# Kernel tuning notes

Measured on AMD Instinct MI355X. Metric: run time of the kernel, lower is better.

Reference implementation:

```python
import jax, jax.numpy as jnp
import numpy as np

N = 80000
E = 1280000
EPS = 1e-5

def _lrelu(x):
    return jax.nn.leaky_relu(x, 0.01)

def _bn(h):
    # training-mode BatchNorm1d with batch size 1: stats over the node dim; affine is identity at init
    return (h - h.mean(0)) / jnp.sqrt(h.var(0) + EPS)

def _ln(h, g, b):
    m = h.mean(-1, keepdims=True)
    v = h.var(-1, keepdims=True)
    return (h - m) / jnp.sqrt(v + EPS) * g + b

def _gcn(h, w, b, src, dst, n):
    # PyG GCNConv: add self loops, symmetric deg^-1/2 normalization, aggregate at target
    hw = h @ w.T
    loop = jnp.arange(n, dtype=src.dtype)
    s = jnp.concatenate([src, loop])
    d = jnp.concatenate([dst, loop])
    deg = jax.ops.segment_sum(jnp.ones(d.shape, hw.dtype), d, num_segments=n)
    dinv = jnp.where(deg > 0, 1.0 / jnp.sqrt(deg), 0.0)
    msg = hw[s] * (dinv[s] * dinv[d])[:, None]  # [E+N, C]
    return jax.ops.segment_sum(msg, d, num_segments=n) + b

def _tnet(x, c1w, c1b, c2w, c2b, c3w, c3b, f1w, f1b, f2w, f2b, f3w, f3b):
    h = jax.nn.relu(x @ c1w.T + c1b)          # [N,64]  (source skips bn1)
    h = jax.nn.relu(_bn(h @ c2w.T + c2b))     # [N,128]
    h = jax.nn.relu(_bn(h @ c3w.T + c3b))     # [N,1024]
    g = h.max(0)                              # global max pool -> [1024]
    g = jax.nn.relu(g @ f1w.T + f1b)
    g = jax.nn.relu(g @ f2w.T + f2b)
    iden = jnp.array([1.0, 0.0, 0.0, 0.0, 1.0, 0.0, 0.0, 0.0, 1.0], x.dtype)
    g = g @ f3w.T + f3b + iden
    return g.reshape(3, 3)

def _forward(edge_index, x, tnet_c1_w, tnet_c1_b, tnet_c2_w, tnet_c2_b, tnet_c3_w, tnet_c3_b, tnet_fc1_w, tnet_fc1_b, tnet_fc2_w, tnet_fc2_b, tnet_fc3_w, tnet_fc3_b, conv1_w, conv1_b, g1_li_w, g1_li_b, g1_gcn_w, g1_gcn_b, g1_ln_g, g1_ln_b, conv2_w, conv2_b, g2_li_w, g2_li_b, g2_gcn_w, g2_gcn_b, g2_ln_g, g2_ln_b, conv3_w, conv3_b, out_w, out_b):
    src, dst = edge_index[0], edge_index[1]
    n = x.shape[0]
    T = _tnet(x, tnet_c1_w, tnet_c1_b, tnet_c2_w, tnet_c2_b, tnet_c3_w, tnet_c3_b, tnet_fc1_w, tnet_fc1_b, tnet_fc2_w, tnet_fc2_b, tnet_fc3_w, tnet_fc3_b)
    h0 = x @ T                                  # [N,3] spatial transform
    xg = _lrelu(h0 @ conv1_w.T + conv1_b)       # [N,64] (conv1d k=1 == per-node linear)
    # Gcn_Attention 1
    nf = _lrelu(xg @ g1_li_w.T + g1_li_b)
    nf2 = _lrelu(_gcn(nf, g1_gcn_w, g1_gcn_b, src, dst, n))
    h = _ln(jnp.concatenate([nf, nf2], 1), g1_ln_g, g1_ln_b)   # [N,128]
    h = _lrelu(h @ conv2_w.T + conv2_b)
    # Gcn_Attention 2
    nf = _lrelu(h @ g2_li_w.T + g2_li_b)
    nf2 = _lrelu(_gcn(nf, g2_gcn_w, g2_gcn_b, src, dst, n))
    h = _ln(jnp.concatenate([nf, nf2], 1), g2_ln_g, g2_ln_b)   # [N,256]
    h = jnp.concatenate([h, xg], 1)                            # [N,320]
    h = _lrelu(h @ conv3_w.T + conv3_b)                        # [N,256]
    pooled = h.mean(0)                                         # global mean pool (single graph)
    feat = jnp.concatenate([jnp.broadcast_to(pooled, (n, pooled.shape[0])), xg], 1)  # [N,320]
    return feat @ out_w.T + out_b                              # [N,4]

def setup_inputs():
    ki = iter(jax.random.split(jax.random.key(0), 32))
    def W(shape):
        return jax.random.normal(next(ki), shape, jnp.float32) * (1.0 / float(np.sqrt(shape[-1])))
    z = lambda n: jnp.zeros((n,), jnp.float32)
    o = lambda n: jnp.ones((n,), jnp.float32)
    inp = {}
    inp['x'] = jax.random.normal(next(ki), (N, 3), jnp.float32)
    inp['edge_index'] = jax.random.randint(next(ki), (2, E), 0, N, dtype=jnp.int32)
    inp['tnet_c1_w'] = W((64, 3)); inp['tnet_c1_b'] = z(64)
    inp['tnet_c2_w'] = W((128, 64)); inp['tnet_c2_b'] = z(128)
    inp['tnet_c3_w'] = W((1024, 128)); inp['tnet_c3_b'] = z(1024)
    inp['tnet_fc1_w'] = W((512, 1024)); inp['tnet_fc1_b'] = z(512)
    inp['tnet_fc2_w'] = W((256, 512)); inp['tnet_fc2_b'] = z(256)
    inp['tnet_fc3_w'] = W((9, 256)); inp['tnet_fc3_b'] = z(9)
    inp['conv1_w'] = W((64, 3)); inp['conv1_b'] = z(64)
    inp['g1_li_w'] = W((64, 64)); inp['g1_li_b'] = z(64)
    inp['g1_gcn_w'] = W((64, 64)); inp['g1_gcn_b'] = z(64)
    inp['g1_ln_g'] = o(128); inp['g1_ln_b'] = z(128)
    inp['conv2_w'] = W((128, 128)); inp['conv2_b'] = z(128)
    inp['g2_li_w'] = W((128, 128)); inp['g2_li_b'] = z(128)
    inp['g2_gcn_w'] = W((128, 128)); inp['g2_gcn_b'] = z(128)
    inp['g2_ln_g'] = o(256); inp['g2_ln_b'] = z(256)
    inp['conv3_w'] = W((256, 320)); inp['conv3_b'] = z(256)
    inp['out_w'] = W((4, 320)); inp['out_b'] = z(4)
    return inp

def reference(x, edge_index, tnet_c1_w, tnet_c1_b, tnet_c2_w, tnet_c2_b, tnet_c3_w, tnet_c3_b, tnet_fc1_w, tnet_fc1_b, tnet_fc2_w, tnet_fc2_b, tnet_fc3_w, tnet_fc3_b, conv1_w, conv1_b, g1_li_w, g1_li_b, g1_gcn_w, g1_gcn_b, g1_ln_g, g1_ln_b, conv2_w, conv2_b, g2_li_w, g2_li_b, g2_gcn_w, g2_gcn_b, g2_ln_g, g2_ln_b, conv3_w, conv3_b, out_w, out_b):
    return _forward(edge_index, x, tnet_c1_w, tnet_c1_b, tnet_c2_w, tnet_c2_b, tnet_c3_w, tnet_c3_b, tnet_fc1_w, tnet_fc1_b, tnet_fc2_w, tnet_fc2_b, tnet_fc3_w, tnet_fc3_b, conv1_w, conv1_b, g1_li_w, g1_li_b, g1_gcn_w, g1_gcn_b, g1_ln_g, g1_ln_b, conv2_w, conv2_b, g2_li_w, g2_li_b, g2_gcn_w, g2_gcn_b, g2_ln_g, g2_ln_b, conv3_w, conv3_b, out_w, out_b)
```

## Files before the change

kernel.cpp:

```cpp
#include <hip/hip_runtime.h>
#include <cstddef>

#define EPSV 1e-5f

typedef __attribute__((ext_vector_type(8))) short frag8;
typedef __attribute__((ext_vector_type(4))) float f32x4;

__device__ __forceinline__ float lrelu01(float v) { return v > 0.f ? v : 0.01f * v; }
__device__ __forceinline__ void atomAddF(float* p, float v) { unsafeAtomicAdd(p, v); }
__device__ __forceinline__ unsigned fkey(float f) {
    unsigned u = __float_as_uint(f);
    return (u & 0x80000000u) ? ~u : (u | 0x80000000u);
}
__device__ __forceinline__ unsigned short f2b(float f) {
    unsigned u = __float_as_uint(f);
    unsigned r = u + 0x7fffu + ((u >> 16) & 1u);
    return (unsigned short)(r >> 16);
}
__device__ __forceinline__ float b2f(unsigned short h) {
    return __uint_as_float(((unsigned)h) << 16);
}
__device__ __forceinline__ float blo(unsigned u) { return __uint_as_float(u << 16); }
__device__ __forceinline__ float bhi(unsigned u) { return __uint_as_float(u & 0xffff0000u); }

static inline unsigned cdivu(unsigned a, unsigned b) { return (a + b - 1) / b; }


__global__ void k_degrank(const int* __restrict__ dst, int* __restrict__ deg,
                          int* __restrict__ rank, int E) {
    int e = blockIdx.x * 256 + threadIdx.x;
    if (e < E) rank[e] = atomicAdd(&deg[dst[e]], 1);
}

__global__ void k_scan_local(const int* __restrict__ deg, int* __restrict__ startv,
                             int* __restrict__ bsum, float* __restrict__ dinv, int n) {
    __shared__ int t0[256];
    int tid = threadIdx.x;
    int i = blockIdx.x * 256 + tid;
    int v = (i < n) ? deg[i] : 0;
    if (i < n) dinv[i] = rsqrtf((float)(v + 1));
    t0[tid] = v;
    __syncthreads();
    for (int o = 1; o < 256; o <<= 1) {
        int add = (tid >= o) ? t0[tid - o] : 0;
        __syncthreads();
        t0[tid] += add;
        __syncthreads();
    }
    if (i < n) startv[i] = t0[tid] - v;
    if (tid == 255) bsum[blockIdx.x] = t0[255];
}

__global__ void k_scan_bsum(int* __restrict__ bsum, int nb) {
    __shared__ int t0[512];
    int tid = threadIdx.x;
    int v = (tid < nb) ? bsum[tid] : 0;
    t0[tid] = v;
    __syncthreads();
    for (int o = 1; o < 512; o <<= 1) {
        int add = (tid >= o) ? t0[tid - o] : 0;
        __syncthreads();
        t0[tid] += add;
        __syncthreads();
    }
    if (tid < nb) bsum[tid] = t0[tid] - v;
}

__global__ void k_scan_add(int* __restrict__ startv, const int* __restrict__ bsum, int n) {
    int i = blockIdx.x * 256 + threadIdx.x;
    if (i < n) startv[i] += bsum[blockIdx.x];
}

__global__ void k_fill(const int* __restrict__ src, const int* __restrict__ dst,
                       const int* __restrict__ rank, const int* __restrict__ startv,
                       int* __restrict__ csr, int E) {
    int e = blockIdx.x * 256 + threadIdx.x;
    if (e < E) csr[startv[dst[e]] + rank[e]] = src[e];
}

template <int CH>
__launch_bounds__(256)
__global__ void k_gln(const int* __restrict__ startv, const int* __restrict__ degv,
                      const int* __restrict__ csr, const unsigned short* __restrict__ q,
                      const unsigned short* __restrict__ nf, const float* __restrict__ dinv,
                      const float* __restrict__ gcn_b, const float* __restrict__ lng,
                      const float* __restrict__ lnb, unsigned short* __restrict__ outp,
                      int ldo, int n) {
    const int wv = threadIdx.x >> 6, lane = threadIdx.x & 63;
    const int g = lane >> 4, p = lane & 15;
    int node = blockIdx.x * 4 + wv;
    if (node >= n) return;
    constexpr int CPL = CH / 16;
    constexpr int DPL = CPL / 2;

    float acc[CPL];
#pragma unroll
    for (int k = 0; k < CPL; ++k) acc[k] = 0.f;

    {
        unsigned su[DPL];
        const unsigned short* qrow = q + (size_t)node * CH + p * CPL;
        if (DPL == 4) *(uint4*)su = *(const uint4*)qrow;
        else          *(uint2*)su = *(const uint2*)qrow;
        if (g == 0) {
#pragma unroll
            for (int d = 0; d < DPL; ++d) { acc[2 * d] += blo(su[d]); acc[2 * d + 1] += bhi(su[d]); }
        }
    }

    int s0 = startv[node], cnt = degv[node];
    int sidx[4];
#pragma unroll
    for (int t = 0; t < 4; ++t) { int j = t * 4 + g; sidx[t] = (j < cnt) ? csr[s0 + j] : 0; }
    for (int j0 = 0; j0 < cnt; j0 += 16) {
        unsigned buf[4][DPL];
#pragma unroll
        for (int t = 0; t < 4; ++t) {
            const unsigned short* src = q + (size_t)sidx[t] * CH + p * CPL;
            if (DPL == 4) *(uint4*)buf[t] = *(const uint4*)src;
            else          *(uint2*)buf[t] = *(const uint2*)src;
        }
        int nsidx[4];
#pragma unroll
        for (int t = 0; t < 4; ++t) {
            int j = j0 + 16 + t * 4 + g;
            nsidx[t] = (j < cnt) ? csr[s0 + j] : 0;
        }
#pragma unroll
        for (int t = 0; t < 4; ++t) {
            if (j0 + t * 4 + g < cnt) {
#pragma unroll
                for (int d = 0; d < DPL; ++d) {
                    acc[2 * d] += blo(buf[t][d]);
                    acc[2 * d + 1] += bhi(buf[t][d]);
                }
            }
        }
#pragma unroll
        for (int t = 0; t < 4; ++t) sidx[t] = nsidx[t];
    }

#pragma unroll
    for (int k = 0; k < CPL; ++k) {
        acc[k] += __shfl_xor(acc[k], 16);
        acc[k] += __shfl_xor(acc[k], 32);
    }

    float di = dinv[node];
    float nv[CPL], bv[CPL];
    {
        unsigned su[DPL];
        const unsigned short* nrow = nf + (size_t)node * CH + p * CPL;
        if (DPL == 4) *(uint4*)su = *(const uint4*)nrow;
        else          *(uint2*)su = *(const uint2*)nrow;
#pragma unroll
        for (int d = 0; d < DPL; ++d) { nv[2 * d] = blo(su[d]); nv[2 * d + 1] = bhi(su[d]); }
    }
    const float* gb = gcn_b + p * CPL;
#pragma unroll
    for (int k = 0; k < CPL; ++k) bv[k] = lrelu01(di * acc[k] + gb[k]);

    float s = 0.f, ss = 0.f;
#pragma unroll
    for (int k = 0; k < CPL; ++k) { s += nv[k] + bv[k]; ss += nv[k] * nv[k] + bv[k] * bv[k]; }
#pragma unroll
    for (int off = 32; off > 0; off >>= 1) { s += __shfl_xor(s, off); ss += __shfl_xor(ss, off); }
    const float inv = 1.f / (float)(8 * CH);
    float mu = s * inv;
    float var = ss * inv - mu * mu;
    float rsg = rsqrtf(var + EPSV);

    unsigned short* orow = outp + (size_t)node * ldo;
    if (g == 0) {
        unsigned short tmp[CPL];
        const float* lg = lng + p * CPL; const float* lb = lnb + p * CPL;
#pragma unroll
        for (int k = 0; k < CPL; ++k) tmp[k] = f2b((nv[k] - mu) * rsg * lg[k] + lb[k]);
        if (DPL == 4) *(uint4*)(orow + p * CPL) = *(uint4*)tmp;
        else          *(uint2*)(orow + p * CPL) = *(uint2*)tmp;
    } else if (g == 1) {
        unsigned short tmp[CPL];
        const float* lg = lng + CH + p * CPL; const float* lb = lnb + CH + p * CPL;
#pragma unroll
        for (int k = 0; k < CPL; ++k) tmp[k] = f2b((bv[k] - mu) * rsg * lg[k] + lb[k]);
        if (DPL == 4) *(uint4*)(orow + CH + p * CPL) = *(uint4*)tmp;
        else          *(uint2*)(orow + CH + p * CPL) = *(uint2*)tmp;
    }
}


__global__ void k_wconv(const float* __restrict__ s0, const float* __restrict__ s1,
                        const float* __restrict__ s2, const float* __restrict__ s3,
                        const float* __restrict__ s4, const float* __restrict__ s5,
                        const float* __restrict__ s6, const float* __restrict__ s7,
                        unsigned short* __restrict__ dst) {
    int t = blockIdx.x * 256 + threadIdx.x;
    if (t >= 278528) return;
    const float* srcs[8] = {s0, s1, s2, s3, s4, s5, s6, s7};
    const int off[9] = {0, 8192, 139264, 143360, 147456, 163840, 180224, 196608, 278528};
    int seg = 0;
    while (t >= off[seg + 1]) ++seg;
    unsigned short v = f2b(srcs[seg][t - off[seg]]);
    if (seg == 1) {
        int li = t - 8192;
        int rch = li >> 7, k = li & 127;
        int cb = rch >> 7, r = rch & 127;
        int flat = ((r >> 4) * 4 + (k >> 5)) * 64 + ((k >> 3) & 3) * 16 + (r & 15);
        dst[8192 + cb * 16384 + flat * 8 + (k & 7)] = v;
    } else {
        dst[t] = v;
    }
}

__global__ void k_h1(const float* __restrict__ x, const float* __restrict__ w,
                     const float* __restrict__ b, unsigned short* __restrict__ h1, int n) {
    int node = blockIdx.x * 256 + threadIdx.x;
    if (node >= n) return;
    float x0 = x[node * 3], x1 = x[node * 3 + 1], x2 = x[node * 3 + 2];
    unsigned short* o = h1 + (size_t)node * 64;
#pragma unroll
    for (int cp = 0; cp < 8; ++cp) {
        unsigned short tmp[8];
#pragma unroll
        for (int t = 0; t < 8; ++t) {
            int c = cp * 8 + t;
            float v = x0 * w[c * 3] + x1 * w[c * 3 + 1] + x2 * w[c * 3 + 2] + b[c];
            tmp[t] = f2b(fmaxf(v, 0.f));
        }
        *(float4*)(o + cp * 8) = *(float4*)tmp;
    }
}

__global__ void k_prebn(const float* __restrict__ z, const float* __restrict__ sum2,
                        const float* __restrict__ ss2, unsigned short* __restrict__ a3f,
                        int n16, float invn) {
    int t = blockIdx.x * 256 + threadIdx.x;
    if (t >= n16) return;
    int row = t >> 4, cp = t & 15;
    int c = cp * 8;
    const float* src = z + (size_t)row * 128 + c;
    float4 v0 = *(const float4*)src;
    float4 v1 = *(const float4*)(src + 4);
    float vv[8] = {v0.x, v0.y, v0.z, v0.w, v1.x, v1.y, v1.z, v1.w};
    unsigned short o[8];
#pragma unroll
    for (int i = 0; i < 8; ++i) {
        float m = sum2[c + i] * invn;
        float var = ss2[c + i] * invn - m * m;
        o[i] = f2b(fmaxf((vv[i] - m) * rsqrtf(var + EPSV), 0.f));
    }
    int tile = row >> 7, r = row & 127;
    int flat = ((r >> 4) * 4 + (cp >> 2)) * 64 + (cp & 3) * 16 + (r & 15);
    *(float4*)(a3f + (size_t)tile * 16384 + flat * 8) = *(float4*)o;
}

__launch_bounds__(256)
__global__ void k_fc1(const float* __restrict__ sum3, const float* __restrict__ ss3,
                      const unsigned* __restrict__ maxk,
                      const float* __restrict__ f1w, const float* __restrict__ f1b,
                      float* __restrict__ a1, float invn) {
    __shared__ float g[1024];
    int tid = threadIdx.x;
    for (int c = tid; c < 1024; c += 256) {
        float m = sum3[c] * invn;
        float var = ss3[c] * invn - m * m;
        unsigned k = maxk[c];
        unsigned u = (k & 0x80000000u) ? (k & 0x7FFFFFFFu) : ~k;
        g[c] = fmaxf((__uint_as_float(u) - m) * rsqrtf(var + EPSV), 0.f);
    }
    __syncthreads();
    int row = blockIdx.x * 64 + (tid >> 2);
    int part = tid & 3;
    const float* w = f1w + (size_t)row * 1024 + part * 256;
    const float* gg = g + part * 256;
    float s = 0.f;
    for (int k = 0; k < 256; ++k) s = fmaf(w[k], gg[k], s);
    s += __shfl_xor(s, 1); s += __shfl_xor(s, 2);
    if (part == 0) a1[row] = fmaxf(s + f1b[row], 0.f);
}

__launch_bounds__(256)
__global__ void k_fc23(const float* __restrict__ a1, const float* __restrict__ f2w,
                       const float* __restrict__ f2b, const float* __restrict__ f3w,
                       const float* __restrict__ f3b, float* __restrict__ T9) {
    __shared__ float a2[256];
    int tid = threadIdx.x;
    {
        const float* w = f2w + (size_t)tid * 512;
        float s = f2b[tid];
        for (int k = 0; k < 512; ++k) s = fmaf(w[k], a1[k], s);
        a2[tid] = fmaxf(s, 0.f);
    }
    __syncthreads();
    if (tid < 9) {
        const float* w = f3w + (size_t)tid * 256;
        float s = f3b[tid];
        for (int k = 0; k < 256; ++k) s = fmaf(w[k], a2[k], s);
        if (tid == 0 || tid == 4 || tid == 8) s += 1.f;
        T9[tid] = s;
    }
}

__global__ void k_xg(const float* __restrict__ x, const float* __restrict__ T9,
                     const float* __restrict__ w, const float* __restrict__ b,
                     unsigned short* __restrict__ xg, int n) {
    int node = blockIdx.x * 256 + threadIdx.x;
    if (node >= n) return;
    float x0 = x[node * 3], x1 = x[node * 3 + 1], x2 = x[node * 3 + 2];
    float h0 = x0 * T9[0] + x1 * T9[3] + x2 * T9[6];
    float h1 = x0 * T9[1] + x1 * T9[4] + x2 * T9[7];
    float h2 = x0 * T9[2] + x1 * T9[5] + x2 * T9[8];
    unsigned short* o = xg + (size_t)node * 320;
#pragma unroll
    for (int cp = 0; cp < 8; ++cp) {
        unsigned short tmp[8];
#pragma unroll
        for (int t = 0; t < 8; ++t) {
            int c = cp * 8 + t;
            float v = h0 * w[c * 3] + h1 * w[c * 3 + 1] + h2 * w[c * 3 + 2] + b[c];
            tmp[t] = f2b(lrelu01(v));
        }
        *(float4*)(o + cp * 8) = *(float4*)tmp;
    }
}

__global__ void k_const4(const float* __restrict__ pooled, const float* __restrict__ ow,
                         const float* __restrict__ ob, float* __restrict__ c4, float invn) {
    int j = threadIdx.x >> 6, lane = threadIdx.x & 63;
    float s = 0.f;
    for (int c = lane; c < 256; c += 64) s += pooled[c] * invn * ow[j * 320 + c];
#pragma unroll
    for (int off = 32; off > 0; off >>= 1) s += __shfl_down(s, off);
    if (lane == 0) c4[j] = s + ob[j];
}

__global__ void k_out(const unsigned short* __restrict__ hcat, const float* __restrict__ ow,
                      const float* __restrict__ c4, float* __restrict__ out, int n) {
    int node = blockIdx.x * 256 + threadIdx.x;
    if (node >= n) return;
    const unsigned short* xgp = hcat + (size_t)node * 320 + 256;
    float s0 = c4[0], s1 = c4[1], s2 = c4[2], s3 = c4[3];
#pragma unroll
    for (int cp = 0; cp < 8; ++cp) {
        float4 raw = *(const float4*)(xgp + cp * 8);
        unsigned short tmp[8];
        *(float4*)tmp = raw;
#pragma unroll
        for (int t = 0; t < 8; ++t) {
            int k = 256 + cp * 8 + t;
            float f = b2f(tmp[t]);
            s0 = fmaf(f, ow[k], s0);
            s1 = fmaf(f, ow[320 + k], s1);
            s2 = fmaf(f, ow[640 + k], s2);
            s3 = fmaf(f, ow[960 + k], s3);
        }
    }
    *(float4*)(out + (size_t)node * 4) = make_float4(s0, s1, s2, s3);
}

enum { MF_BIAS = 1, MF_LRELU = 2, MF_DINV = 4, MF_STOREF = 8, MF_STOREB = 16,
       MF_STATS = 32, MF_COLSUM = 64 };

template <int BN, int MODE>
__launch_bounds__(256)
__global__ void k_mgemm(const unsigned short* __restrict__ A, int lda, int K,
                        const unsigned short* __restrict__ W,
                        const float* __restrict__ bias,
                        float* __restrict__ OutF, unsigned short* __restrict__ OutB, int ldo,
                        const float* __restrict__ dinv,
                        float* __restrict__ sum_o, float* __restrict__ ss_o,
                        unsigned* __restrict__ maxk_o) {
    constexpr int BM = 128;
    constexpr int LDT = 40;
    __shared__ unsigned short As[BM * LDT];
    __shared__ unsigned short Ws[BN * LDT];
    __shared__ float redS[2 * 128];
    __shared__ unsigned redM[128];

    const int tid = threadIdx.x;
    const int wid = tid >> 6, lane = tid & 63;
    const int quad = lane >> 4, lrow = lane & 15;
    const int bn0 = blockIdx.x * BM;
    const int bc0 = blockIdx.y * BN;

    constexpr int NI = (BN == 128) ? 4 : 2;
    constexpr int NJ = 4;
    const int wm = (BN == 128) ? (wid & 1) * 64 : wid * 32;
    const int wn = (BN == 128) ? (wid >> 1) * 64 : 0;

    if (MODE & (MF_STATS | MF_COLSUM)) {
        for (int c = tid; c < BN; c += 256) {
            redS[c] = 0.f; redS[128 + c] = 0.f; redM[c] = 0u;
        }
    }

    f32x4 acc[NI][NJ] = {};

    for (int k0 = 0; k0 < K; k0 += 32) {
#pragma unroll
        for (int h = 0; h < 2; ++h) {
            int ch = tid + h * 256;
            int row = ch >> 2, cp = ch & 3;
            const unsigned short* src = A + (size_t)(bn0 + row) * lda + k0 + cp * 8;
            *(float4*)&As[row * LDT + cp * 8] = *(const float4*)src;
        }
#pragma unroll
        for (int h = 0; h < BN / 64; ++h) {
            int ch = tid + h * 256;
            int row = ch >> 2, cp = ch & 3;
            const unsigned short* src = W + (size_t)(bc0 + row) * K + k0 + cp * 8;
            *(float4*)&Ws[row * LDT + cp * 8] = *(const float4*)src;
        }
        __syncthreads();
        frag8 af[NI], bf[NJ];
#pragma unroll
        for (int i = 0; i < NI; ++i)
            af[i] = *(const frag8*)&As[(wm + i * 16 + lrow) * LDT + quad * 8];
#pragma unroll
        for (int j = 0; j < NJ; ++j)
            bf[j] = *(const frag8*)&Ws[(wn + j * 16 + lrow) * LDT + quad * 8];
#pragma unroll
        for (int i = 0; i < NI; ++i)
#pragma unroll
            for (int j = 0; j < NJ; ++j)
                acc[i][j] = __builtin_amdgcn_mfma_f32_16x16x32_bf16(af[i], bf[j], acc[i][j], 0, 0, 0);
        __syncthreads();
    }

#pragma unroll
    for (int j = 0; j < NJ; ++j) {
        const int col = bc0 + wn + j * 16 + lrow;
        float bv = (MODE & MF_BIAS) ? bias[col] : 0.f;
        float s = 0.f, q = 0.f, m = -3.4e38f;
#pragma unroll
        for (int i = 0; i < NI; ++i) {
            const int rowb = bn0 + wm + i * 16 + quad * 4;
#pragma unroll
            for (int r = 0; r < 4; ++r) {
                float t = acc[i][j][r] + bv;
                if (MODE & MF_LRELU) t = lrelu01(t);
                if (MODE & MF_DINV) t *= dinv[rowb + r];
                if (MODE & MF_STOREF) OutF[(size_t)(rowb + r) * ldo + col] = t;
                if (MODE & MF_STOREB) OutB[(size_t)(rowb + r) * ldo + col] = f2b(t);
                s += t; q += t * t; m = fmaxf(m, t);
            }
        }
        if (MODE & (MF_STATS | MF_COLSUM)) {
            s += __shfl_xor(s, 16); s += __shfl_xor(s, 32);
            if (MODE & MF_STATS) {
                q += __shfl_xor(q, 16); q += __shfl_xor(q, 32);
                m = fmaxf(m, __shfl_xor(m, 16)); m = fmaxf(m, __shfl_xor(m, 32));
            }
            if (quad == 0) {
                int lc = wn + j * 16 + lrow;
                atomicAdd(&redS[lc], s);
                if (MODE & MF_STATS) {
                    atomicAdd(&redS[128 + lc], q);
                    atomicMax(&redM[lc], fkey(m));
                }
            }
        }
    }
    if (MODE & (MF_STATS | MF_COLSUM)) {
        __syncthreads();
        for (int c = tid; c < BN; c += 256) {
            atomAddF(&sum_o[bc0 + c], redS[c]);
            if (MODE & MF_STATS) {
                atomAddF(&ss_o[bc0 + c], redS[128 + c]);
                atomicMax(&maxk_o[bc0 + c], redM[c]);
            }
        }
    }
}

template <int BN>
__launch_bounds__(256)
__global__ void k_ligc(const unsigned short* __restrict__ A, int lda, int K,
                       const unsigned short* __restrict__ Wli, const float* __restrict__ bli,
                       const unsigned short* __restrict__ Wgc, const float* __restrict__ dinv,
                       unsigned short* __restrict__ NF, int ldnf,
                       unsigned short* __restrict__ Q, int ldq) {
    constexpr int BM = 128;
    constexpr int LDT = 40;
    constexpr int LDT2 = BN + 8;
    __shared__ unsigned short SA[BM * LDT2];
    __shared__ unsigned short Ws[BN * LDT];

    const int tid = threadIdx.x;
    const int wid = tid >> 6, lane = tid & 63;
    const int quad = lane >> 4, lrow = lane & 15;
    const int bn0 = blockIdx.x * BM;
    constexpr int NI = (BN == 128) ? 4 : 2;
    constexpr int NJ = 4;
    const int wm = (BN == 128) ? (wid & 1) * 64 : wid * 32;
    const int wn = (BN == 128) ? (wid >> 1) * 64 : 0;

    {
        f32x4 acc[NI][NJ] = {};
        for (int k0 = 0; k0 < K; k0 += 32) {
#pragma unroll
            for (int h = 0; h < 2; ++h) {
                int ch = tid + h * 256;
                int row = ch >> 2, cp = ch & 3;
                *(float4*)&SA[row * LDT + cp * 8] =
                    *(const float4*)(A + (size_t)(bn0 + row) * lda + k0 + cp * 8);
            }
#pragma unroll
            for (int h = 0; h < BN / 64; ++h) {
                int ch = tid + h * 256;
                int row = ch >> 2, cp = ch & 3;
                *(float4*)&Ws[row * LDT + cp * 8] =
                    *(const float4*)(Wli + (size_t)row * K + k0 + cp * 8);
            }
            __syncthreads();
            frag8 af[NI], bf[NJ];
#pragma unroll
            for (int i = 0; i < NI; ++i)
                af[i] = *(const frag8*)&SA[(wm + i * 16 + lrow) * LDT + quad * 8];
#pragma unroll
            for (int j = 0; j < NJ; ++j)
                bf[j] = *(const frag8*)&Ws[(wn + j * 16 + lrow) * LDT + quad * 8];
#pragma unroll
            for (int i = 0; i < NI; ++i)
#pragma unroll
                for (int j = 0; j < NJ; ++j)
                    acc[i][j] = __builtin_amdgcn_mfma_f32_16x16x32_bf16(af[i], bf[j], acc[i][j], 0, 0, 0);
            __syncthreads();
        }
#pragma unroll
        for (int j = 0; j < NJ; ++j) {
            const int col = wn + j * 16 + lrow;
            float bv = bli[col];
#pragma unroll
            for (int i = 0; i < NI; ++i) {
                const int rowl = wm + i * 16 + quad * 4;
#pragma unroll
                for (int r = 0; r < 4; ++r) {
                    unsigned short h = f2b(lrelu01(acc[i][j][r] + bv));
                    NF[(size_t)(bn0 + rowl + r) * ldnf + col] = h;
                    SA[(rowl + r) * LDT2 + col] = h;
                }
            }
        }
        __syncthreads();
    }
    {
        f32x4 acc[NI][NJ] = {};
        for (int k0 = 0; k0 < BN; k0 += 32) {
#pragma unroll
            for (int h = 0; h < BN / 64; ++h) {
                int ch = tid + h * 256;
                int row = ch >> 2, cp = ch & 3;
                *(float4*)&Ws[row * LDT + cp * 8] =
                    *(const float4*)(Wgc + (size_t)row * BN + k0 + cp * 8);
            }
            __syncthreads();
            frag8 af[NI], bf[NJ];
#pragma unroll
            for (int i = 0; i < NI; ++i)
                af[i] = *(const frag8*)&SA[(wm + i * 16 + lrow) * LDT2 + k0 + quad * 8];
#pragma unroll
            for (int j = 0; j < NJ; ++j)
                bf[j] = *(const frag8*)&Ws[(wn + j * 16 + lrow) * LDT + quad * 8];
#pragma unroll
            for (int i = 0; i < NI; ++i)
#pragma unroll
                for (int j = 0; j < NJ; ++j)
                    acc[i][j] = __builtin_amdgcn_mfma_f32_16x16x32_bf16(af[i], bf[j], acc[i][j], 0, 0, 0);
            __syncthreads();
        }
#pragma unroll
        for (int j = 0; j < NJ; ++j) {
            const int col = wn + j * 16 + lrow;
#pragma unroll
            for (int i = 0; i < NI; ++i) {
                const int rowb = bn0 + wm + i * 16 + quad * 4;
#pragma unroll
                for (int r = 0; r < 4; ++r) {
                    float t = acc[i][j][r] * dinv[rowb + r];
                    Q[(size_t)(rowb + r) * ldq + col] = f2b(t);
                }
            }
        }
    }
}

__launch_bounds__(256)
__global__ void k_z3(const unsigned short* __restrict__ AF,
                     const unsigned short* __restrict__ WF,
                     const float* __restrict__ bias,
                     float* __restrict__ sum_o, float* __restrict__ ss_o,
                     unsigned* __restrict__ maxk_o, int ntiles) {
    const int tid = threadIdx.x;
    const int wid = tid >> 6, lane = tid & 63;
    const int quad = lane >> 4, lrow = lane & 15;

    int bid = blockIdx.x;
    int w = (bid & 7) * ntiles + (bid >> 3);
    const int tile = w >> 3;
    const int cb = w & 7;
    const unsigned short* At = AF + (size_t)tile * 16384;
    const unsigned short* Wt = WF + (size_t)cb * 16384;

    const int ar = (wid & 1) * 4;
    const int wc = (wid >> 1) * 4;
    f32x4 acc[4][4] = {};
#pragma unroll
    for (int kc = 0; kc < 4; ++kc) {
        frag8 af[4], bf[4];
#pragma unroll
        for (int i = 0; i < 4; ++i)
            af[i] = *(const frag8*)&At[(((ar + i) * 4 + kc) * 64 + lane) * 8];
#pragma unroll
        for (int j = 0; j < 4; ++j)
            bf[j] = *(const frag8*)&Wt[(((wc + j) * 4 + kc) * 64 + lane) * 8];
#pragma unroll
        for (int i = 0; i < 4; ++i)
#pragma unroll
            for (int j = 0; j < 4; ++j)
                acc[i][j] = __builtin_amdgcn_mfma_f32_16x16x32_bf16(af[i], bf[j], acc[i][j], 0, 0, 0);
    }

#pragma unroll
    for (int j = 0; j < 4; ++j) {
        int c = cb * 128 + (wc + j) * 16 + lrow;
        float bv = bias[c];
        float s = 0.f, q = 0.f, m = -3.4e38f;
#pragma unroll
        for (int i = 0; i < 4; ++i)
#pragma unroll
            for (int r = 0; r < 4; ++r) {
                float t = acc[i][j][r] + bv;
                s += t; q += t * t; m = fmaxf(m, t);
            }
        s += __shfl_xor(s, 16); s += __shfl_xor(s, 32);
        q += __shfl_xor(q, 16); q += __shfl_xor(q, 32);
        m = fmaxf(m, __shfl_xor(m, 16)); m = fmaxf(m, __shfl_xor(m, 32));
        if (quad == 0) {
            atomAddF(&sum_o[c], s);
            atomAddF(&ss_o[c], q);
            atomicMax(&maxk_o[c], fkey(m));
        }
    }
}


extern "C" void kernel_launch(void* const* d_in, const int* in_sizes, int n_in,
                              void* d_out, int out_size, void* d_ws, size_t ws_size,
                              hipStream_t stream) {
    const float* x   = (const float*)d_in[0];
    const int*   ei  = (const int*)d_in[1];
    const float* c1w = (const float*)d_in[2];  const float* c1b = (const float*)d_in[3];
    const float* c2w = (const float*)d_in[4];  const float* c2b = (const float*)d_in[5];
    const float* c3w = (const float*)d_in[6];  const float* c3b = (const float*)d_in[7];
    const float* f1w = (const float*)d_in[8];  const float* f1b = (const float*)d_in[9];
    const float* f2w = (const float*)d_in[10]; const float* f2b = (const float*)d_in[11];
    const float* f3w = (const float*)d_in[12]; const float* f3b = (const float*)d_in[13];
    const float* cv1w = (const float*)d_in[14]; const float* cv1b = (const float*)d_in[15];
    const float* li1w = (const float*)d_in[16]; const float* li1b = (const float*)d_in[17];
    const float* gc1w = (const float*)d_in[18]; const float* gc1b = (const float*)d_in[19];
    const float* ln1g = (const float*)d_in[20]; const float* ln1b = (const float*)d_in[21];
    const float* cv2w = (const float*)d_in[22]; const float* cv2b = (const float*)d_in[23];
    const float* li2w = (const float*)d_in[24]; const float* li2b = (const float*)d_in[25];
    const float* gc2w = (const float*)d_in[26]; const float* gc2b = (const float*)d_in[27];
    const float* ln2g = (const float*)d_in[28]; const float* ln2b = (const float*)d_in[29];
    const float* cv3w = (const float*)d_in[30]; const float* cv3b = (const float*)d_in[31];
    const float* ow  = (const float*)d_in[32]; const float* ob  = (const float*)d_in[33];
    float* out = (float*)d_out;

    const int N = in_sizes[0] / 3;
    const int E = in_sizes[1] / 2;
    const int* srcI = ei;
    const int* dstI = ei + E;

    char* base = (char*)d_ws;
    size_t off = 0;
    auto take = [&](size_t bytes) -> char* {
        char* p = base + off;
        off = (off + bytes + 255) & ~(size_t)255;
        return p;
    };
    int*   deg    = (int*)  take((size_t)N * 4);
    float* dinv   = (float*)take((size_t)N * 4);
    int*   startv = (int*)  take((size_t)N * 4);
    int*   rank   = (int*)  take((size_t)E * 4);
    int*   csr    = (int*)  take((size_t)E * 4);
    int*   bsum   = (int*)  take(512 * 4);
    float* sm     = (float*)take(8192 * 4);
    unsigned short* WB = (unsigned short*)take(278528 * 2);
    unsigned short* H  = (unsigned short*)take((size_t)N * 320 * 2);
    float* F1 = (float*)take((size_t)N * 128 * 4);
    unsigned short* B1 = (unsigned short*)take((size_t)N * 64 * 2);
    unsigned short* B2 = (unsigned short*)take((size_t)N * 128 * 2);
    unsigned short* B3 = (unsigned short*)take((size_t)N * 128 * 2);

    unsigned short* c2wb  = WB + 0;
    unsigned short* c3wf  = WB + 8192;
    unsigned short* li1wb = WB + 139264;
    unsigned short* gc1wb = WB + 143360;
    unsigned short* cv2wb = WB + 147456;
    unsigned short* li2wb = WB + 163840;
    unsigned short* gc2wb = WB + 180224;
    unsigned short* cv3wb = WB + 196608;

    float* sum2 = sm + 0;    float* ss2 = sm + 128;
    float* sum3 = sm + 256;  float* ss3 = sm + 1280;
    unsigned* maxk = (unsigned*)(sm + 2304);
    float* pooled = sm + 3328;
    unsigned* dmax = (unsigned*)(sm + 3584);
    float* T9  = sm + 3968; float* c4 = sm + 3984;
    float* a1  = sm + 5120;

    const float invn = 1.0f / (float)N;
    const dim3 blk(256);
    const unsigned GX = (unsigned)(N / 128);
    const unsigned NB = cdivu((unsigned)N, 256);

    hipMemsetAsync(deg, 0, (size_t)N * 4, stream);
    hipMemsetAsync(sm, 0, 3712 * 4, stream);

    k_degrank<<<cdivu(E, 256), blk, 0, stream>>>(dstI, deg, rank, E);
    k_scan_local<<<NB, blk, 0, stream>>>(deg, startv, bsum, dinv, N);
    k_scan_bsum<<<1, 512, 0, stream>>>(bsum, (int)NB);
    k_scan_add<<<NB, blk, 0, stream>>>(startv, bsum, N);
    k_fill<<<cdivu(E, 256), blk, 0, stream>>>(srcI, dstI, rank, startv, csr, E);

    k_wconv<<<cdivu(278528, 256), blk, 0, stream>>>(c2w, c3w, li1w, gc1w, cv2w, li2w, gc2w, cv3w, WB);

    k_h1<<<cdivu((unsigned)N, 256), blk, 0, stream>>>(x, c1w, c1b, B1, N);
    k_mgemm<128, (MF_BIAS | MF_STOREF | MF_STATS)><<<dim3(GX, 1), blk, 0, stream>>>(
        B1, 64, 64, c2wb, c2b, F1, nullptr, 128, nullptr, sum2, ss2, dmax);
    k_prebn<<<cdivu((unsigned)N * 16, 256), blk, 0, stream>>>(F1, sum2, ss2, B2, N * 16, invn);
    k_z3<<<8 * GX, blk, 0, stream>>>(B2, c3wf, c3b, sum3, ss3, maxk, (int)GX);
    k_fc1<<<8, blk, 0, stream>>>(sum3, ss3, maxk, f1w, f1b, a1, invn);
    k_fc23<<<1, blk, 0, stream>>>(a1, f2w, f2b, f3w, f3b, T9);
    k_xg<<<cdivu((unsigned)N, 256), blk, 0, stream>>>(x, T9, cv1w, cv1b, H + 256, N);

    k_ligc<64><<<GX, blk, 0, stream>>>(H + 256, 320, 64, li1wb, li1b, gc1wb, dinv, B1, 64, B2, 64);
    k_gln<64><<<cdivu((unsigned)N, 4), blk, 0, stream>>>(
        startv, deg, csr, B2, B1, dinv, gc1b, ln1g, ln1b, B3, 128, N);
    k_mgemm<128, (MF_BIAS | MF_LRELU | MF_STOREB)><<<dim3(GX, 1), blk, 0, stream>>>(
        B3, 128, 128, cv2wb, cv2b, nullptr, B2, 128, nullptr, nullptr, nullptr, nullptr);

    k_ligc<128><<<GX, blk, 0, stream>>>(B2, 128, 128, li2wb, li2b, gc2wb, dinv, B3, 128, B2, 128);
    k_gln<128><<<cdivu((unsigned)N, 4), blk, 0, stream>>>(
        startv, deg, csr, B2, B3, dinv, gc2b, ln2g, ln2b, H, 320, N);

    k_mgemm<128, (MF_BIAS | MF_LRELU | MF_COLSUM)><<<dim3(GX, 2), blk, 0, stream>>>(
        H, 320, 320, cv3wb, cv3b, nullptr, nullptr, 0, nullptr, pooled, nullptr, nullptr);

    k_const4<<<1, 256, 0, stream>>>(pooled, ow, ob, c4, invn);
    k_out<<<cdivu((unsigned)N, 256), blk, 0, stream>>>(H, ow, c4, out, N);
}
```

Before: 548.9 us.

## Merge independent preprocessing kernels into fused multi-role launches

Independent stages (CSR build steps, weight conversion, T-Net stages, head FCs) are packed into combined kernels that pick their role by block index. This cuts the launch count and lets unrelated work overlap inside one grid. The fc1/fc2/fc3 head is fused into one block, the const4 and out kernels are merged, and the conv3 GEMM grid is swapped so both column halves of a row tile run next to each other. The risks are a slow single-block head, block-index dispatch overhead, and the added memsets on B2 padding.

Measured after the change: 587.5 us. +7.0%, slower.

```diff
diff --git a/kernel.cpp b/kernel.cpp
--- a/kernel.cpp
+++ b/kernel.cpp
@@ -26,17 +26,17 @@
 static inline unsigned cdivu(unsigned a, unsigned b) { return (a + b - 1) / b; }
 
 
-__global__ void k_degrank(const int* __restrict__ dst, int* __restrict__ deg,
-                          int* __restrict__ rank, int E) {
-    int e = blockIdx.x * 256 + threadIdx.x;
+__device__ void degrank_body(int bid, const int* __restrict__ dst, int* __restrict__ deg,
+                             int* __restrict__ rank, int E) {
+    int e = bid * 256 + threadIdx.x;
     if (e < E) rank[e] = atomicAdd(&deg[dst[e]], 1);
 }
 
-__global__ void k_scan_local(const int* __restrict__ deg, int* __restrict__ startv,
-                             int* __restrict__ bsum, float* __restrict__ dinv, int n) {
+__device__ void scan_local_body(int bid, const int* __restrict__ deg, int* __restrict__ startv,
+                                int* __restrict__ bsum, float* __restrict__ dinv, int n) {
     __shared__ int t0[256];
     int tid = threadIdx.x;
-    int i = blockIdx.x * 256 + tid;
+    int i = bid * 256 + tid;
     int v = (i < n) ? deg[i] : 0;
     if (i < n) dinv[i] = rsqrtf((float)(v + 1));
     t0[tid] = v;
@@ -48,153 +48,47 @@
         __syncthreads();
     }
     if (i < n) startv[i] = t0[tid] - v;
-    if (tid == 255) bsum[blockIdx.x] = t0[255];
-}
-
-__global__ void k_scan_bsum(int* __restrict__ bsum, int nb) {
+    if (tid == 255) bsum[bid] = t0[255];
+}
+
+__device__ void scan_bsum_body(int* __restrict__ bsum, int nb) {
     __shared__ int t0[512];
+    __shared__ int t1[512];
     int tid = threadIdx.x;
-    int v = (tid < nb) ? bsum[tid] : 0;
-    t0[tid] = v;
+    int v0 = (tid < nb) ? bsum[tid] : 0;
+    int v1 = (tid + 256 < nb) ? bsum[tid + 256] : 0;
+    t0[tid] = v0; t0[tid + 256] = v1;
     __syncthreads();
+    int* a = t0; int* b = t1;
     for (int o = 1; o < 512; o <<= 1) {
-        int add = (tid >= o) ? t0[tid - o] : 0;
+        b[tid]       = a[tid]       + ((tid >= o)       ? a[tid - o]       : 0);
+        b[tid + 256] = a[tid + 256] + ((tid + 256 >= o) ? a[tid + 256 - o] : 0);
         __syncthreads();
-        t0[tid] += add;
-        __syncthreads();
-    }
-    if (tid < nb) bsum[tid] = t0[tid] - v;
-}
-
-__global__ void k_scan_add(int* __restrict__ startv, const int* __restrict__ bsum, int n) {
-    int i = blockIdx.x * 256 + threadIdx.x;
-    if (i < n) startv[i] += bsum[blockIdx.x];
-}
-
-__global__ void k_fill(const int* __restrict__ src, const int* __restrict__ dst,
-                       const int* __restrict__ rank, const int* __restrict__ startv,
-                       int* __restrict__ csr, int E) {
-    int e = blockIdx.x * 256 + threadIdx.x;
+        int* t = a; a = b; b = t;
+    }
+    if (tid < nb) bsum[tid] = a[tid] - v0;
+    if (tid + 256 < nb) bsum[tid + 256] = a[tid + 256] - v1;
+}
+
+__device__ void scan_add_body(int bid, int* __restrict__ startv, const int* __restrict__ bsum, int n) {
+    int i = bid * 256 + threadIdx.x;
+    if (i < n) startv[i] += bsum[bid];
+}
+
+__device__ void fill_body(int bid, const int* __restrict__ src, const int* __restrict__ dst,
+                          const int* __restrict__ rank, const int* __restrict__ startv,
+                          int* __restrict__ csr, int E) {
+    int e = bid * 256 + threadIdx.x;
     if (e < E) csr[startv[dst[e]] + rank[e]] = src[e];
 }
 
-template <int CH>
-__launch_bounds__(256)
-__global__ void k_gln(const int* __restrict__ startv, const int* __restrict__ degv,
-                      const int* __restrict__ csr, const unsigned short* __restrict__ q,
-                      const unsigned short* __restrict__ nf, const float* __restrict__ dinv,
-                      const float* __restrict__ gcn_b, const float* __restrict__ lng,
-                      const float* __restrict__ lnb, unsigned short* __restrict__ outp,
-                      int ldo, int n) {
-    const int wv = threadIdx.x >> 6, lane = threadIdx.x & 63;
-    const int g = lane >> 4, p = lane & 15;
-    int node = blockIdx.x * 4 + wv;
-    if (node >= n) return;
-    constexpr int CPL = CH / 16;
-    constexpr int DPL = CPL / 2;
-
-    float acc[CPL];
-#pragma unroll
-    for (int k = 0; k < CPL; ++k) acc[k] = 0.f;
-
-    {
-        unsigned su[DPL];
-        const unsigned short* qrow = q + (size_t)node * CH + p * CPL;
-        if (DPL == 4) *(uint4*)su = *(const uint4*)qrow;
-        else          *(uint2*)su = *(const uint2*)qrow;
-        if (g == 0) {
-#pragma unroll
-            for (int d = 0; d < DPL; ++d) { acc[2 * d] += blo(su[d]); acc[2 * d + 1] += bhi(su[d]); }
-        }
-    }
-
-    int s0 = startv[node], cnt = degv[node];
-    int sidx[4];
-#pragma unroll
-    for (int t = 0; t < 4; ++t) { int j = t * 4 + g; sidx[t] = (j < cnt) ? csr[s0 + j] : 0; }
-    for (int j0 = 0; j0 < cnt; j0 += 16) {
-        unsigned buf[4][DPL];
-#pragma unroll
-        for (int t = 0; t < 4; ++t) {
-            const unsigned short* src = q + (size_t)sidx[t] * CH + p * CPL;
-            if (DPL == 4) *(uint4*)buf[t] = *(const uint4*)src;
-            else          *(uint2*)buf[t] = *(const uint2*)src;
-        }
-        int nsidx[4];
-#pragma unroll
-        for (int t = 0; t < 4; ++t) {
-            int j = j0 + 16 + t * 4 + g;
-            nsidx[t] = (j < cnt) ? csr[s0 + j] : 0;
-        }
-#pragma unroll
-        for (int t = 0; t < 4; ++t) {
-            if (j0 + t * 4 + g < cnt) {
-#pragma unroll
-                for (int d = 0; d < DPL; ++d) {
-                    acc[2 * d] += blo(buf[t][d]);
-                    acc[2 * d + 1] += bhi(buf[t][d]);
-                }
-            }
-        }
-#pragma unroll
-        for (int t = 0; t < 4; ++t) sidx[t] = nsidx[t];
-    }
-
-#pragma unroll
-    for (int k = 0; k < CPL; ++k) {
-        acc[k] += __shfl_xor(acc[k], 16);
-        acc[k] += __shfl_xor(acc[k], 32);
-    }
-
-    float di = dinv[node];
-    float nv[CPL], bv[CPL];
-    {
-        unsigned su[DPL];
-        const unsigned short* nrow = nf + (size_t)node * CH + p * CPL;
-        if (DPL == 4) *(uint4*)su = *(const uint4*)nrow;
-        else          *(uint2*)su = *(const uint2*)nrow;
-#pragma unroll
-        for (int d = 0; d < DPL; ++d) { nv[2 * d] = blo(su[d]); nv[2 * d + 1] = bhi(su[d]); }
-    }
-    const float* gb = gcn_b + p * CPL;
-#pragma unroll
-    for (int k = 0; k < CPL; ++k) bv[k] = lrelu01(di * acc[k] + gb[k]);
-
-    float s = 0.f, ss = 0.f;
-#pragma unroll
-    for (int k = 0; k < CPL; ++k) { s += nv[k] + bv[k]; ss += nv[k] * nv[k] + bv[k] * bv[k]; }
-#pragma unroll
-    for (int off = 32; off > 0; off >>= 1) { s += __shfl_xor(s, off); ss += __shfl_xor(ss, off); }
-    const float inv = 1.f / (float)(8 * CH);
-    float mu = s * inv;
-    float var = ss * inv - mu * mu;
-    float rsg = rsqrtf(var + EPSV);
-
-    unsigned short* orow = outp + (size_t)node * ldo;
-    if (g == 0) {
-        unsigned short tmp[CPL];
-        const float* lg = lng + p * CPL; const float* lb = lnb + p * CPL;
-#pragma unroll
-        for (int k = 0; k < CPL; ++k) tmp[k] = f2b((nv[k] - mu) * rsg * lg[k] + lb[k]);
-        if (DPL == 4) *(uint4*)(orow + p * CPL) = *(uint4*)tmp;
-        else          *(uint2*)(orow + p * CPL) = *(uint2*)tmp;
-    } else if (g == 1) {
-        unsigned short tmp[CPL];
-        const float* lg = lng + CH + p * CPL; const float* lb = lnb + CH + p * CPL;
-#pragma unroll
-        for (int k = 0; k < CPL; ++k) tmp[k] = f2b((bv[k] - mu) * rsg * lg[k] + lb[k]);
-        if (DPL == 4) *(uint4*)(orow + CH + p * CPL) = *(uint4*)tmp;
-        else          *(uint2*)(orow + CH + p * CPL) = *(uint2*)tmp;
-    }
-}
-
-
-__global__ void k_wconv(const float* __restrict__ s0, const float* __restrict__ s1,
-                        const float* __restrict__ s2, const float* __restrict__ s3,
-                        const float* __restrict__ s4, const float* __restrict__ s5,
-                        const float* __restrict__ s6, const float* __restrict__ s7,
-                        unsigned short* __restrict__ dst) {
-    int t = blockIdx.x * 256 + threadIdx.x;
+
+__device__ void wconv_body(int bid, const float* __restrict__ s0, const float* __restrict__ s1,
+                           const float* __restrict__ s2, const float* __restrict__ s3,
+                           const float* __restrict__ s4, const float* __restrict__ s5,
+                           const float* __restrict__ s6, const float* __restrict__ s7,
+                           unsigned short* __restrict__ dst) {
+    int t = bid * 256 + threadIdx.x;
     if (t >= 278528) return;
     const float* srcs[8] = {s0, s1, s2, s3, s4, s5, s6, s7};
     const int off[9] = {0, 8192, 139264, 143360, 147456, 163840, 180224, 196608, 278528};
@@ -212,9 +106,9 @@
     }
 }
 
-__global__ void k_h1(const float* __restrict__ x, const float* __restrict__ w,
-                     const float* __restrict__ b, unsigned short* __restrict__ h1, int n) {
-    int node = blockIdx.x * 256 + threadIdx.x;
+__device__ void h1_body(int bid, const float* __restrict__ x, const float* __restrict__ w,
+                        const float* __restrict__ b, unsigned short* __restrict__ h1, int n) {
+    int node = bid * 256 + threadIdx.x;
     if (node >= n) return;
     float x0 = x[node * 3], x1 = x[node * 3 + 1], x2 = x[node * 3 + 2];
     unsigned short* o = h1 + (size_t)node * 64;
@@ -231,10 +125,10 @@
     }
 }
 
-__global__ void k_prebn(const float* __restrict__ z, const float* __restrict__ sum2,
-                        const float* __restrict__ ss2, unsigned short* __restrict__ a3f,
-                        int n16, float invn) {
-    int t = blockIdx.x * 256 + threadIdx.x;
+__device__ void prebn_body(int bid, const float* __restrict__ z, const float* __restrict__ sum2,
+                           const float* __restrict__ ss2, unsigned short* __restrict__ a3f,
+                           int n16, float invn) {
+    int t = bid * 256 + threadIdx.x;
     if (t >= n16) return;
     int row = t >> 4, cp = t & 15;
     int c = cp * 8;
@@ -254,12 +148,15 @@
     *(float4*)(a3f + (size_t)tile * 16384 + flat * 8) = *(float4*)o;
 }
 
-__launch_bounds__(256)
-__global__ void k_fc1(const float* __restrict__ sum3, const float* __restrict__ ss3,
-                      const unsigned* __restrict__ maxk,
-                      const float* __restrict__ f1w, const float* __restrict__ f1b,
-                      float* __restrict__ a1, float invn) {
+__device__ void head_body(const float* __restrict__ sum3, const float* __restrict__ ss3,
+                          const unsigned* __restrict__ maxk,
+                          const float* __restrict__ f1w, const float* __restrict__ f1b,
+                          const float* __restrict__ f2w, const float* __restrict__ f2b,
+                          const float* __restrict__ f3w, const float* __restrict__ f3b,
+                          float* __restrict__ T9, float invn) {
     __shared__ float g[1024];
+    __shared__ float a1[512];
+    __shared__ float a2[256];
     int tid = threadIdx.x;
     for (int c = tid; c < 1024; c += 256) {
         float m = sum3[c] * invn;
@@ -269,22 +166,22 @@
         g[c] = fmaxf((__uint_as_float(u) - m) * rsqrtf(var + EPSV), 0.f);
     }
     __syncthreads();
-    int row = blockIdx.x * 64 + (tid >> 2);
-    int part = tid & 3;
-    const float* w = f1w + (size_t)row * 1024 + part * 256;
-    const float* gg = g + part * 256;
-    float s = 0.f;
-    for (int k = 0; k < 256; ++k) s = fmaf(w[k], gg[k], s);
-    s += __shfl_xor(s, 1); s += __shfl_xor(s, 2);
-    if (part == 0) a1[row] = fmaxf(s + f1b[row], 0.f);
-}
-
-__launch_bounds__(256)
-__global__ void k_fc23(const float* __restrict__ a1, const float* __restrict__ f2w,
-                       const float* __restrict__ f2b, const float* __restrict__ f3w,
-                       const float* __restrict__ f3b, float* __restrict__ T9) {
-    __shared__ float a2[256];
-    int tid = threadIdx.x;
+#pragma unroll
+    for (int h = 0; h < 2; ++h) {
+        int r = tid + h * 256;
+        const float* w = f1w + (size_t)r * 1024;
+        float sp[4];
+#pragma unroll
+        for (int part = 0; part < 4; ++part) {
+            float s = 0.f;
+            const float* wp = w + part * 256;
+            const float* gp = g + part * 256;
+            for (int k = 0; k < 256; ++k) s = fmaf(wp[k], gp[k], s);
+            sp[part] = s;
+        }
+        a1[r] = fmaxf(((sp[0] + sp[1]) + (sp[2] + sp[3])) + f1b[r], 0.f);
+    }
+    __syncthreads();
     {
         const float* w = f2w + (size_t)tid * 512;
         float s = f2b[tid];
@@ -300,6 +197,360 @@
         T9[tid] = s;
     }
 }
+
+enum { MF_BIAS = 1, MF_LRELU = 2, MF_DINV = 4, MF_STOREF = 8, MF_STOREB = 16,
+       MF_STATS = 32, MF_COLSUM = 64 };
+
+template <int BN, int MODE>
+__device__ void mgemm_body(int bx, int by,
+                           const unsigned short* __restrict__ A, int lda, int K,
+                           const unsigned short* __restrict__ W,
+                           const float* __restrict__ bias,
+                           float* __restrict__ OutF, unsigned short* __restrict__ OutB, int ldo,
+                           const float* __restrict__ dinv,
+                           float* __restrict__ sum_o, float* __restrict__ ss_o,
+                           unsigned* __restrict__ maxk_o) {
+    constexpr int BM = 128;
+    constexpr int LDT = 40;
+    __shared__ unsigned short As[BM * LDT];
+    __shared__ unsigned short Ws[BN * LDT];
+    __shared__ float redS[2 * 128];
+    __shared__ unsigned redM[128];
+
+    const int tid = threadIdx.x;
+    const int wid = tid >> 6, lane = tid & 63;
+    const int quad = lane >> 4, lrow = lane & 15;
+    const int bn0 = bx * BM;
+    const int bc0 = by * BN;
+
+    constexpr int NI = (BN == 128) ? 4 : 2;
+    constexpr int NJ = 4;
+    const int wm = (BN == 128) ? (wid & 1) * 64 : wid * 32;
+    const int wn = (BN == 128) ? (wid >> 1) * 64 : 0;
+
+    if (MODE & (MF_STATS | MF_COLSUM)) {
+        for (int c = tid; c < BN; c += 256) {
+            redS[c] = 0.f; redS[128 + c] = 0.f; redM[c] = 0u;
+        }
+    }
+
+    f32x4 acc[NI][NJ] = {};
+
+    for (int k0 = 0; k0 < K; k0 += 32) {
+#pragma unroll
+        for (int h = 0; h < 2; ++h) {
+            int ch = tid + h * 256;
+            int row = ch >> 2, cp = ch & 3;
+            const unsigned short* src = A + (size_t)(bn0 + row) * lda + k0 + cp * 8;
+            *(float4*)&As[row * LDT + cp * 8] = *(const float4*)src;
+        }
+#pragma unroll
+        for (int h = 0; h < BN / 64; ++h) {
+            int ch = tid + h * 256;
+            int row = ch >> 2, cp = ch & 3;
+            const unsigned short* src = W + (size_t)(bc0 + row) * K + k0 + cp * 8;
+            *(float4*)&Ws[row * LDT + cp * 8] = *(const float4*)src;
+        }
+        __syncthreads();
+        frag8 af[NI], bf[NJ];
+#pragma unroll
+        for (int i = 0; i < NI; ++i)
+            af[i] = *(const frag8*)&As[(wm + i * 16 + lrow) * LDT + quad * 8];
+#pragma unroll
+        for (int j = 0; j < NJ; ++j)
+            bf[j] = *(const frag8*)&Ws[(wn + j * 16 + lrow) * LDT + quad * 8];
+#pragma unroll
+        for (int i = 0; i < NI; ++i)
+#pragma unroll
+            for (int j = 0; j < NJ; ++j)
+                acc[i][j] = __builtin_amdgcn_mfma_f32_16x16x32_bf16(af[i], bf[j], acc[i][j], 0, 0, 0);
+        __syncthreads();
+    }
+
+#pragma unroll
+    for (int j = 0; j < NJ; ++j) {
+        const int col = bc0 + wn + j * 16 + lrow;
+        float bv = (MODE & MF_BIAS) ? bias[col] : 0.f;
+        float s = 0.f, q = 0.f, m = -3.4e38f;
+#pragma unroll
+        for (int i = 0; i < NI; ++i) {
+            const int rowb = bn0 + wm + i * 16 + quad * 4;
+#pragma unroll
+            for (int r = 0; r < 4; ++r) {
+                float t = acc[i][j][r] + bv;
+                if (MODE & MF_LRELU) t = lrelu01(t);
+                if (MODE & MF_DINV) t *= dinv[rowb + r];
+                if (MODE & MF_STOREF) OutF[(size_t)(rowb + r) * ldo + col] = t;
+                if (MODE & MF_STOREB) OutB[(size_t)(rowb + r) * ldo + col] = f2b(t);
+                s += t; q += t * t; m = fmaxf(m, t);
+            }
+        }
+        if (MODE & (MF_STATS | MF_COLSUM)) {
+            s += __shfl_xor(s, 16); s += __shfl_xor(s, 32);
+            if (MODE & MF_STATS) {
+                q += __shfl_xor(q, 16); q += __shfl_xor(q, 32);
+                m = fmaxf(m, __shfl_xor(m, 16)); m = fmaxf(m, __shfl_xor(m, 32));
+            }
+            if (quad == 0) {
+                int lc = wn + j * 16 + lrow;
+                atomicAdd(&redS[lc], s);
+                if (MODE & MF_STATS) {
+                    atomicAdd(&redS[128 + lc], q);
+                    atomicMax(&redM[lc], fkey(m));
+                }
+            }
+        }
+    }
+    if (MODE & (MF_STATS | MF_COLSUM)) {
+        __syncthreads();
+        for (int c = tid; c < BN; c += 256) {
+            atomAddF(&sum_o[bc0 + c], redS[c]);
+            if (MODE & MF_STATS) {
+                atomAddF(&ss_o[bc0 + c], redS[128 + c]);
+                atomicMax(&maxk_o[bc0 + c], redM[c]);
+            }
+        }
+    }
+}
+
+template <int BN, int MODE, int SWAP>
+__launch_bounds__(256)
+__global__ void k_mgemm(const unsigned short* __restrict__ A, int lda, int K,
+                        const unsigned short* __restrict__ W,
+                        const float* __restrict__ bias,
+                        float* __restrict__ OutF, unsigned short* __restrict__ OutB, int ldo,
+                        const float* __restrict__ dinv,
+                        float* __restrict__ sum_o, float* __restrict__ ss_o,
+                        unsigned* __restrict__ maxk_o) {
+    int bx = SWAP ? blockIdx.y : blockIdx.x;
+    int by = SWAP ? blockIdx.x : blockIdx.y;
+    mgemm_body<BN, MODE>(bx, by, A, lda, K, W, bias, OutF, OutB, ldo, dinv, sum_o, ss_o, maxk_o);
+}
+
+__device__ void z3_body(int bid,
+                        const unsigned short* __restrict__ AF,
+                        const unsigned short* __restrict__ WF,
+                        const float* __restrict__ bias,
+                        float* __restrict__ sum_o, float* __restrict__ ss_o,
+                        unsigned* __restrict__ maxk_o, int ntiles) {
+    const int tid = threadIdx.x;
+    const int wid = tid >> 6, lane = tid & 63;
+    const int quad = lane >> 4, lrow = lane & 15;
+
+    int w = (bid & 7) * ntiles + (bid >> 3);
+    const int tile = w >> 3;
+    const int cb = w & 7;
+    const unsigned short* At = AF + (size_t)tile * 16384;
+    const unsigned short* Wt = WF + (size_t)cb * 16384;
+
+    const int ar = (wid & 1) * 4;
+    const int wc = (wid >> 1) * 4;
+    f32x4 acc[4][4] = {};
+#pragma unroll
+    for (int kc = 0; kc < 4; ++kc) {
+        frag8 af[4], bf[4];
+#pragma unroll
+        for (int i = 0; i < 4; ++i)
+            af[i] = *(const frag8*)&At[(((ar + i) * 4 + kc) * 64 + lane) * 8];
+#pragma unroll
+        for (int j = 0; j < 4; ++j)
+            bf[j] = *(const frag8*)&Wt[(((wc + j) * 4 + kc) * 64 + lane) * 8];
+#pragma unroll
+        for (int i = 0; i < 4; ++i)
+#pragma unroll
+            for (int j = 0; j < 4; ++j)
+                acc[i][j] = __builtin_amdgcn_mfma_f32_16x16x32_bf16(af[i], bf[j], acc[i][j], 0, 0, 0);
+    }
+
+#pragma unroll
+    for (int j = 0; j < 4; ++j) {
+        int c = cb * 128 + (wc + j) * 16 + lrow;
+        float bv = bias[c];
+        float s = 0.f, q = 0.f, m = -3.4e38f;
+#pragma unroll
+        for (int i = 0; i < 4; ++i)
+#pragma unroll
+            for (int r = 0; r < 4; ++r) {
+                float t = acc[i][j][r] + bv;
+                s += t; q += t * t; m = fmaxf(m, t);
+            }
+        s += __shfl_xor(s, 16); s += __shfl_xor(s, 32);
+        q += __shfl_xor(q, 16); q += __shfl_xor(q, 32);
+        m = fmaxf(m, __shfl_xor(m, 16)); m = fmaxf(m, __shfl_xor(m, 32));
+        if (quad == 0) {
+            atomAddF(&sum_o[c], s);
+            atomAddF(&ss_o[c], q);
+            atomicMax(&maxk_o[c], fkey(m));
+        }
+    }
+}
+
+
+__launch_bounds__(256)
+__global__ void FK1(const int* __restrict__ dst, int* __restrict__ deg, int* __restrict__ rank,
+                    int E, int EB,
+                    const float* s0, const float* s1, const float* s2, const float* s3,
+                    const float* s4, const float* s5, const float* s6, const float* s7,
+                    unsigned short* __restrict__ WB, int WCB,
+                    const float* __restrict__ x, const float* __restrict__ c1w,
+                    const float* __restrict__ c1b, unsigned short* __restrict__ B1, int n) {
+    int b = blockIdx.x;
+    if (b < EB) { degrank_body(b, dst, deg, rank, E); return; }
+    b -= EB;
+    if (b < WCB) { wconv_body(b, s0, s1, s2, s3, s4, s5, s6, s7, WB); return; }
+    b -= WCB;
+    h1_body(b, x, c1w, c1b, B1, n);
+}
+
+__launch_bounds__(256)
+__global__ void FK2(const unsigned short* __restrict__ A, int lda, int K,
+                    const unsigned short* __restrict__ W, const float* __restrict__ bias,
+                    float* __restrict__ OutF, int ldo,
+                    float* __restrict__ sum_o, float* __restrict__ ss_o,
+                    unsigned* __restrict__ maxk_o, int GXz,
+                    const int* __restrict__ deg, int* __restrict__ startv,
+                    int* __restrict__ bsum, float* __restrict__ dinvv, int n) {
+    if ((int)blockIdx.x < GXz)
+        mgemm_body<128, (MF_BIAS | MF_STOREF | MF_STATS)>(
+            blockIdx.x, 0, A, lda, K, W, bias, OutF, nullptr, ldo, nullptr, sum_o, ss_o, maxk_o);
+    else
+        scan_local_body(blockIdx.x - GXz, deg, startv, bsum, dinvv, n);
+}
+
+__launch_bounds__(256)
+__global__ void FK3(const float* __restrict__ z, const float* __restrict__ sum2,
+                    const float* __restrict__ ss2, unsigned short* __restrict__ a3f,
+                    int n16, float invn, int PB, int* __restrict__ bsum, int nb) {
+    if ((int)blockIdx.x < PB) prebn_body(blockIdx.x, z, sum2, ss2, a3f, n16, invn);
+    else scan_bsum_body(bsum, nb);
+}
+
+__launch_bounds__(256)
+__global__ void FK4(const unsigned short* __restrict__ AF, const unsigned short* __restrict__ WF,
+                    const float* __restrict__ bias,
+                    float* __restrict__ sum_o, float* __restrict__ ss_o,
+                    unsigned* __restrict__ maxk_o, int ntiles, int NZ,
+                    int* __restrict__ startv, const int* __restrict__ bsum, int n) {
+    if ((int)blockIdx.x < NZ) z3_body(blockIdx.x, AF, WF, bias, sum_o, ss_o, maxk_o, ntiles);
+    else scan_add_body(blockIdx.x - NZ, startv, bsum, n);
+}
+
+__launch_bounds__(256)
+__global__ void FK5(const int* __restrict__ src, const int* __restrict__ dst,
+                    const int* __restrict__ rank, const int* __restrict__ startv,
+                    int* __restrict__ csr, int E, int EB,
+                    const float* __restrict__ sum3, const float* __restrict__ ss3,
+                    const unsigned* __restrict__ maxk,
+                    const float* __restrict__ f1w, const float* __restrict__ f1b,
+                    const float* __restrict__ f2w, const float* __restrict__ f2b,
+                    const float* __restrict__ f3w, const float* __restrict__ f3b,
+                    float* __restrict__ T9, float invn) {
+    if ((int)blockIdx.x < EB) fill_body(blockIdx.x, src, dst, rank, startv, csr, E);
+    else head_body(sum3, ss3, maxk, f1w, f1b, f2w, f2b, f3w, f3b, T9, invn);
+}
+
+template <int CH>
+__launch_bounds__(256)
+__global__ void k_gln(const int* __restrict__ startv, const int* __restrict__ degv,
+                      const int* __restrict__ csr, const unsigned short* __restrict__ q,
+                      const unsigned short* __restrict__ nf, const float* __restrict__ dinv,
+                      const float* __restrict__ gcn_b, const float* __restrict__ lng,
+                      const float* __restrict__ lnb, unsigned short* __restrict__ outp,
+                      int ldo, int n) {
+    constexpr int GRP = (CH == 64) ? 8 : 4;
+    constexpr int PL  = 64 / GRP;
+    constexpr int TT  = 16 / GRP;
+    constexpr int CPL = CH / PL;
+    const int wv = threadIdx.x >> 6, lane = threadIdx.x & 63;
+    const int g = lane / PL, p = lane & (PL - 1);
+    int node = blockIdx.x * 4 + wv;
+    if (node >= n) return;
+
+    const unsigned short* qp = q + (size_t)p * CPL;
+
+    float acc[CPL];
+    {
+        uint4 v = *(const uint4*)(qp + (size_t)node * CH);
+        unsigned sv[4] = {v.x, v.y, v.z, v.w};
+        if (g == 0) {
+#pragma unroll
+            for (int d = 0; d < 4; ++d) { acc[2 * d] = blo(sv[d]); acc[2 * d + 1] = bhi(sv[d]); }
+        } else {
+#pragma unroll
+            for (int k = 0; k < CPL; ++k) acc[k] = 0.f;
+        }
+    }
+
+    int s0 = startv[node], cnt = degv[node];
+    const int* cs = csr + s0;
+    int sidx[TT];
+#pragma unroll
+    for (int t = 0; t < TT; ++t) { int j = t * GRP + g; sidx[t] = (j < cnt) ? cs[j] : n; }
+    for (int j0 = 0; j0 < cnt; j0 += 16) {
+        uint4 buf[TT];
+#pragma unroll
+        for (int t = 0; t < TT; ++t)
+            buf[t] = *(const uint4*)(qp + (size_t)(unsigned)sidx[t] * CH);
+#pragma unroll
+        for (int t = 0; t < TT; ++t) {
+            int j = j0 + 16 + t * GRP + g;
+            sidx[t] = (j < cnt) ? cs[j] : n;
+        }
+#pragma unroll
+        for (int t = 0; t < TT; ++t) {
+            unsigned bw[4] = {buf[t].x, buf[t].y, buf[t].z, buf[t].w};
+#pragma unroll
+            for (int d = 0; d < 4; ++d) {
+                acc[2 * d] += blo(bw[d]);
+                acc[2 * d + 1] += bhi(bw[d]);
+            }
+        }
+    }
+
+#pragma unroll
+    for (int k = 0; k < CPL; ++k) {
+#pragma unroll
+        for (int off = PL; off < 64; off <<= 1) acc[k] += __shfl_xor(acc[k], off);
+    }
+
+    float di = dinv[node];
+    float nv[CPL], bv[CPL];
+    {
+        uint4 v = *(const uint4*)(nf + (size_t)node * CH + p * CPL);
+        unsigned sv[4] = {v.x, v.y, v.z, v.w};
+#pragma unroll
+        for (int d = 0; d < 4; ++d) { nv[2 * d] = blo(sv[d]); nv[2 * d + 1] = bhi(sv[d]); }
+    }
+    const float* gb = gcn_b + p * CPL;
+#pragma unroll
+    for (int k = 0; k < CPL; ++k) bv[k] = lrelu01(di * acc[k] + gb[k]);
+
+    float s = 0.f, ss = 0.f;
+#pragma unroll
+    for (int k = 0; k < CPL; ++k) { s += nv[k] + bv[k]; ss += nv[k] * nv[k] + bv[k] * bv[k]; }
+#pragma unroll
+    for (int off = 32; off > 0; off >>= 1) { s += __shfl_xor(s, off); ss += __shfl_xor(ss, off); }
+    const float inv = 1.f / (float)(GRP * 2 * CH);
+    float mu = s * inv;
+    float var = ss * inv - mu * mu;
+    float rsg = rsqrtf(var + EPSV);
+
+    unsigned short* orow = outp + (size_t)node * ldo;
+    if (g == 0) {
+        unsigned short tmp[CPL];
+        const float* lg = lng + p * CPL; const float* lb = lnb + p * CPL;
+#pragma unroll
+        for (int k = 0; k < CPL; ++k) tmp[k] = f2b((nv[k] - mu) * rsg * lg[k] + lb[k]);
+        *(uint4*)(orow + p * CPL) = *(uint4*)tmp;
+    } else if (g == 1) {
+        unsigned short tmp[CPL];
+        const float* lg = lng + CH + p * CPL; const float* lb = lnb + CH + p * CPL;
+#pragma unroll
+        for (int k = 0; k < CPL; ++k) tmp[k] = f2b((bv[k] - mu) * rsg * lg[k] + lb[k]);
+        *(uint4*)(orow + CH + p * CPL) = *(uint4*)tmp;
+    }
+}
+
 
 __global__ void k_xg(const float* __restrict__ x, const float* __restrict__ T9,
                      const float* __restrict__ w, const float* __restrict__ b,
@@ -321,155 +572,6 @@
             tmp[t] = f2b(lrelu01(v));
         }
         *(float4*)(o + cp * 8) = *(float4*)tmp;
-    }
-}
-
-__global__ void k_const4(const float* __restrict__ pooled, const float* __restrict__ ow,
-                         const float* __restrict__ ob, float* __restrict__ c4, float invn) {
-    int j = threadIdx.x >> 6, lane = threadIdx.x & 63;
-    float s = 0.f;
-    for (int c = lane; c < 256; c += 64) s += pooled[c] * invn * ow[j * 320 + c];
-#pragma unroll
-    for (int off = 32; off > 0; off >>= 1) s += __shfl_down(s, off);
-    if (lane == 0) c4[j] = s + ob[j];
-}
-
-__global__ void k_out(const unsigned short* __restrict__ hcat, const float* __restrict__ ow,
-                      const float* __restrict__ c4, float* __restrict__ out, int n) {
-    int node = blockIdx.x * 256 + threadIdx.x;
-    if (node >= n) return;
-    const unsigned short* xgp = hcat + (size_t)node * 320 + 256;
-    float s0 = c4[0], s1 = c4[1], s2 = c4[2], s3 = c4[3];
-#pragma unroll
-    for (int cp = 0; cp < 8; ++cp) {
-        float4 raw = *(const float4*)(xgp + cp * 8);
-        unsigned short tmp[8];
-        *(float4*)tmp = raw;
-#pragma unroll
-        for (int t = 0; t < 8; ++t) {
-            int k = 256 + cp * 8 + t;
-            float f = b2f(tmp[t]);
-            s0 = fmaf(f, ow[k], s0);
-            s1 = fmaf(f, ow[320 + k], s1);
-            s2 = fmaf(f, ow[640 + k], s2);
-            s3 = fmaf(f, ow[960 + k], s3);
-        }
-    }
-    *(float4*)(out + (size_t)node * 4) = make_float4(s0, s1, s2, s3);
-}
-
-enum { MF_BIAS = 1, MF_LRELU = 2, MF_DINV = 4, MF_STOREF = 8, MF_STOREB = 16,
-       MF_STATS = 32, MF_COLSUM = 64 };
-
-template <int BN, int MODE>
-__launch_bounds__(256)
-__global__ void k_mgemm(const unsigned short* __restrict__ A, int lda, int K,
-                        const unsigned short* __restrict__ W,
-                        const float* __restrict__ bias,
-                        float* __restrict__ OutF, unsigned short* __restrict__ OutB, int ldo,
-                        const float* __restrict__ dinv,
-                        float* __restrict__ sum_o, float* __restrict__ ss_o,
-                        unsigned* __restrict__ maxk_o) {
-    constexpr int BM = 128;
-    constexpr int LDT = 40;
-    __shared__ unsigned short As[BM * LDT];
-    __shared__ unsigned short Ws[BN * LDT];
-    __shared__ float redS[2 * 128];
-    __shared__ unsigned redM[128];
-
-    const int tid = threadIdx.x;
-    const int wid = tid >> 6, lane = tid & 63;
-    const int quad = lane >> 4, lrow = lane & 15;
-    const int bn0 = blockIdx.x * BM;
-    const int bc0 = blockIdx.y * BN;
-
-    constexpr int NI = (BN == 128) ? 4 : 2;
-    constexpr int NJ = 4;
-    const int wm = (BN == 128) ? (wid & 1) * 64 : wid * 32;
-    const int wn = (BN == 128) ? (wid >> 1) * 64 : 0;
-
-    if (MODE & (MF_STATS | MF_COLSUM)) {
-        for (int c = tid; c < BN; c += 256) {
-            redS[c] = 0.f; redS[128 + c] = 0.f; redM[c] = 0u;
-        }
-    }
-
-    f32x4 acc[NI][NJ] = {};
-
-    for (int k0 = 0; k0 < K; k0 += 32) {
-#pragma unroll
-        for (int h = 0; h < 2; ++h) {
-            int ch = tid + h * 256;
-            int row = ch >> 2, cp = ch & 3;
-            const unsigned short* src = A + (size_t)(bn0 + row) * lda + k0 + cp * 8;
-            *(float4*)&As[row * LDT + cp * 8] = *(const float4*)src;
-        }
-#pragma unroll
-        for (int h = 0; h < BN / 64; ++h) {
-            int ch = tid + h * 256;
-            int row = ch >> 2, cp = ch & 3;
-            const unsigned short* src = W + (size_t)(bc0 + row) * K + k0 + cp * 8;
-            *(float4*)&Ws[row * LDT + cp * 8] = *(const float4*)src;
-        }
-        __syncthreads();
-        frag8 af[NI], bf[NJ];
-#pragma unroll
-        for (int i = 0; i < NI; ++i)
-            af[i] = *(const frag8*)&As[(wm + i * 16 + lrow) * LDT + quad * 8];
-#pragma unroll
-        for (int j = 0; j < NJ; ++j)
-            bf[j] = *(const frag8*)&Ws[(wn + j * 16 + lrow) * LDT + quad * 8];
-#pragma unroll
-        for (int i = 0; i < NI; ++i)
-#pragma unroll
-            for (int j = 0; j < NJ; ++j)
-                acc[i][j] = __builtin_amdgcn_mfma_f32_16x16x32_bf16(af[i], bf[j], acc[i][j], 0, 0, 0);
-        __syncthreads();
-    }
-
-#pragma unroll
-    for (int j = 0; j < NJ; ++j) {
-        const int col = bc0 + wn + j * 16 + lrow;
-        float bv = (MODE & MF_BIAS) ? bias[col] : 0.f;
-        float s = 0.f, q = 0.f, m = -3.4e38f;
-#pragma unroll
-        for (int i = 0; i < NI; ++i) {
-            const int rowb = bn0 + wm + i * 16 + quad * 4;
-#pragma unroll
-            for (int r = 0; r < 4; ++r) {
-                float t = acc[i][j][r] + bv;
-                if (MODE & MF_LRELU) t = lrelu01(t);
-                if (MODE & MF_DINV) t *= dinv[rowb + r];
-                if (MODE & MF_STOREF) OutF[(size_t)(rowb + r) * ldo + col] = t;
-                if (MODE & MF_STOREB) OutB[(size_t)(rowb + r) * ldo + col] = f2b(t);
-                s += t; q += t * t; m = fmaxf(m, t);
-            }
-        }
-        if (MODE & (MF_STATS | MF_COLSUM)) {
-            s += __shfl_xor(s, 16); s += __shfl_xor(s, 32);
-            if (MODE & MF_STATS) {
-                q += __shfl_xor(q, 16); q += __shfl_xor(q, 32);
-                m = fmaxf(m, __shfl_xor(m, 16)); m = fmaxf(m, __shfl_xor(m, 32));
-            }
-            if (quad == 0) {
-                int lc = wn + j * 16 + lrow;
-                atomicAdd(&redS[lc], s);
-                if (MODE & MF_STATS) {
-                    atomicAdd(&redS[128 + lc], q);
-                    atomicMax(&redM[lc], fkey(m));
-                }
-            }
-        }
-    }
-    if (MODE & (MF_STATS | MF_COLSUM)) {
-        __syncthreads();
-        for (int c = tid; c < BN; c += 256) {
-            atomAddF(&sum_o[bc0 + c], redS[c]);
-            if (MODE & MF_STATS) {
-                atomAddF(&ss_o[bc0 + c], redS[128 + c]);
-                atomicMax(&maxk_o[bc0 + c], redM[c]);
-            }
-        }
     }
 }
 
@@ -585,63 +687,40 @@
     }
 }
 
-__launch_bounds__(256)
-__global__ void k_z3(const unsigned short* __restrict__ AF,
-                     const unsigned short* __restrict__ WF,
-                     const float* __restrict__ bias,
-                     float* __restrict__ sum_o, float* __restrict__ ss_o,
-                     unsigned* __restrict__ maxk_o, int ntiles) {
-    const int tid = threadIdx.x;
-    const int wid = tid >> 6, lane = tid & 63;
-    const int quad = lane >> 4, lrow = lane & 15;
-
-    int bid = blockIdx.x;
-    int w = (bid & 7) * ntiles + (bid >> 3);
-    const int tile = w >> 3;
-    const int cb = w & 7;
-    const unsigned short* At = AF + (size_t)tile * 16384;
-    const unsigned short* Wt = WF + (size_t)cb * 16384;
-
-    const int ar = (wid & 1) * 4;
-    const int wc = (wid >> 1) * 4;
-    f32x4 acc[4][4] = {};
-#pragma unroll
-    for (int kc = 0; kc < 4; ++kc) {
-        frag8 af[4], bf[4];
-#pragma unroll
-        for (int i = 0; i < 4; ++i)
-            af[i] = *(const frag8*)&At[(((ar + i) * 4 + kc) * 64 + lane) * 8];
-#pragma unroll
-        for (int j = 0; j < 4; ++j)
-            bf[j] = *(const frag8*)&Wt[(((wc + j) * 4 + kc) * 64 + lane) * 8];
-#pragma unroll
-        for (int i = 0; i < 4; ++i)
-#pragma unroll
-            for (int j = 0; j < 4; ++j)
-                acc[i][j] = __builtin_amdgcn_mfma_f32_16x16x32_bf16(af[i], bf[j], acc[i][j], 0, 0, 0);
-    }
-
-#pragma unroll
-    for (int j = 0; j < 4; ++j) {
-        int c = cb * 128 + (wc + j) * 16 + lrow;
-        float bv = bias[c];
-        float s = 0.f, q = 0.f, m = -3.4e38f;
-#pragma unroll
-        for (int i = 0; i < 4; ++i)
-#pragma unroll
-            for (int r = 0; r < 4; ++r) {
-                float t = acc[i][j][r] + bv;
-                s += t; q += t * t; m = fmaxf(m, t);
-            }
-        s += __shfl_xor(s, 16); s += __shfl_xor(s, 32);
-        q += __shfl_xor(q, 16); q += __shfl_xor(q, 32);
-        m = fmaxf(m, __shfl_xor(m, 16)); m = fmaxf(m, __shfl_xor(m, 32));
-        if (quad == 0) {
-            atomAddF(&sum_o[c], s);
-            atomAddF(&ss_o[c], q);
-            atomicMax(&maxk_o[c], fkey(m));
-        }
-    }
+__global__ void k_out2(const unsigned short* __restrict__ hcat, const float* __restrict__ ow,
+                       const float* __restrict__ ob, const float* __restrict__ pooled,
+                       float* __restrict__ out, int n, float invn) {
+    __shared__ float c4s[4];
+    int tid = threadIdx.x;
+    {
+        int j = tid >> 6, lane = tid & 63;
+        float s = 0.f;
+        for (int c = lane; c < 256; c += 64) s += pooled[c] * invn * ow[j * 320 + c];
+#pragma unroll
+        for (int off = 32; off > 0; off >>= 1) s += __shfl_down(s, off);
+        if (lane == 0) c4s[j] = s + ob[j];
+    }
+    __syncthreads();
+    int node = blockIdx.x * 256 + tid;
+    if (node >= n) return;
+    const unsigned short* xgp = hcat + (size_t)node * 320 + 256;
+    float s0 = c4s[0], s1 = c4s[1], s2 = c4s[2], s3 = c4s[3];
+#pragma unroll
+    for (int cp = 0; cp < 8; ++cp) {
+        float4 raw = *(const float4*)(xgp + cp * 8);
+        unsigned short tmp[8];
+        *(float4*)tmp = raw;
+#pragma unroll
+        for (int t = 0; t < 8; ++t) {
+            int k = 256 + cp * 8 + t;
+            float f = b2f(tmp[t]);
+            s0 = fmaf(f, ow[k], s0);
+            s1 = fmaf(f, ow[320 + k], s1);
+            s2 = fmaf(f, ow[640 + k], s2);
+            s3 = fmaf(f, ow[960 + k], s3);
+        }
+    }
+    *(float4*)(out + (size_t)node * 4) = make_float4(s0, s1, s2, s3);
 }
 
 
@@ -691,7 +770,7 @@
     unsigned short* H  = (unsigned short*)take((size_t)N * 320 * 2);
     float* F1 = (float*)take((size_t)N * 128 * 4);
     unsigned short* B1 = (unsigned short*)take((size_t)N * 64 * 2);
-    unsigned short* B2 = (unsigned short*)take((size_t)N * 128 * 2);
+    unsigned short* B2 = (unsigned short*)take(((size_t)N * 128 + 128) * 2);
     unsigned short* B3 = (unsigned short*)take((size_t)N * 128 * 2);
 
     unsigned short* c2wb  = WB + 0;
@@ -708,47 +787,46 @@
     unsigned* maxk = (unsigned*)(sm + 2304);
     float* pooled = sm + 3328;
     unsigned* dmax = (unsigned*)(sm + 3584);
-    float* T9  = sm + 3968; float* c4 = sm + 3984;
-    float* a1  = sm + 5120;
+    float* T9  = sm + 3968;
 
     const float invn = 1.0f / (float)N;
     const dim3 blk(256);
     const unsigned GX = (unsigned)(N / 128);
     const unsigned NB = cdivu((unsigned)N, 256);
+    const unsigned EB = cdivu((unsigned)E, 256);
+    const unsigned WCB = cdivu(278528u, 256);
+    const unsigned PB = cdivu((unsigned)N * 16, 256);
 
     hipMemsetAsync(deg, 0, (size_t)N * 4, stream);
     hipMemsetAsync(sm, 0, 3712 * 4, stream);
-
-    k_degrank<<<cdivu(E, 256), blk, 0, stream>>>(dstI, deg, rank, E);
-    k_scan_local<<<NB, blk, 0, stream>>>(deg, startv, bsum, dinv, N);
-    k_scan_bsum<<<1, 512, 0, stream>>>(bsum, (int)NB);
-    k_scan_add<<<NB, blk, 0, stream>>>(startv, bsum, N);
-    k_fill<<<cdivu(E, 256), blk, 0, stream>>>(srcI, dstI, rank, startv, csr, E);
-
-    k_wconv<<<cdivu(278528, 256), blk, 0, stream>>>(c2w, c3w, li1w, gc1w, cv2w, li2w, gc2w, cv3w, WB);
-
-    k_h1<<<cdivu((unsigned)N, 256), blk, 0, stream>>>(x, c1w, c1b, B1, N);
-    k_mgemm<128, (MF_BIAS | MF_STOREF | MF_STATS)><<<dim3(GX, 1), blk, 0, stream>>>(
-        B1, 64, 64, c2wb, c2b, F1, nullptr, 128, nullptr, sum2, ss2, dmax);
-    k_prebn<<<cdivu((unsigned)N * 16, 256), blk, 0, stream>>>(F1, sum2, ss2, B2, N * 16, invn);
-    k_z3<<<8 * GX, blk, 0, stream>>>(B2, c3wf, c3b, sum3, ss3, maxk, (int)GX);
-    k_fc1<<<8, blk, 0, stream>>>(sum3, ss3, maxk, f1w, f1b, a1, invn);
-    k_fc23<<<1, blk, 0, stream>>>(a1, f2w, f2b, f3w, f3b, T9);
-    k_xg<<<cdivu((unsigned)N, 256), blk, 0, stream>>>(x, T9, cv1w, cv1b, H + 256, N);
+    hipMemsetAsync(B2 + (size_t)N * 128, 0, 256, stream);
+
+    FK1<<<EB + WCB + NB, blk, 0, stream>>>(dstI, deg, rank, E, (int)EB,
+                                           c2w, c3w, li1w, gc1w, cv2w, li2w, gc2w, cv3w,
+                                           WB, (int)WCB, x, c1w, c1b, B1, N);
+    FK2<<<GX + NB, blk, 0, stream>>>(B1, 64, 64, c2wb, c2b, F1, 128,
+                                     sum2, ss2, dmax, (int)GX, deg, startv, bsum, dinv, N);
+    FK3<<<PB + 1, blk, 0, stream>>>(F1, sum2, ss2, B2, N * 16, invn, (int)PB, bsum, (int)NB);
+    FK4<<<8 * GX + NB, blk, 0, stream>>>(B2, c3wf, c3b, sum3, ss3, maxk, (int)GX,
+                                         (int)(8 * GX), startv, bsum, N);
+    hipMemsetAsync(B2 + (size_t)N * 64, 0, 128, stream);
+    FK5<<<EB + 1, blk, 0, stream>>>(srcI, dstI, rank, startv, csr, E, (int)EB,
+                                    sum3, ss3, maxk, f1w, f1b, f2w, f2b, f3w, f3b, T9, invn);
+
+    k_xg<<<NB, blk, 0, stream>>>(x, T9, cv1w, cv1b, H + 256, N);
 
     k_ligc<64><<<GX, blk, 0, stream>>>(H + 256, 320, 64, li1wb, li1b, gc1wb, dinv, B1, 64, B2, 64);
     k_gln<64><<<cdivu((unsigned)N, 4), blk, 0, stream>>>(
         startv, deg, csr, B2, B1, dinv, gc1b, ln1g, ln1b, B3, 128, N);
-    k_mgemm<128, (MF_BIAS | MF_LRELU | MF_STOREB)><<<dim3(GX, 1), blk, 0, stream>>>(
+    k_mgemm<128, (MF_BIAS | MF_LRELU | MF_STOREB), 0><<<dim3(GX, 1), blk, 0, stream>>>(
         B3, 128, 128, cv2wb, cv2b, nullptr, B2, 128, nullptr, nullptr, nullptr, nullptr);
 
     k_ligc<128><<<GX, blk, 0, stream>>>(B2, 128, 128, li2wb, li2b, gc2wb, dinv, B3, 128, B2, 128);
     k_gln<128><<<cdivu((unsigned)N, 4), blk, 0, stream>>>(
         startv, deg, csr, B2, B3, dinv, gc2b, ln2g, ln2b, H, 320, N);
 
-    k_mgemm<128, (MF_BIAS | MF_LRELU | MF_COLSUM)><<<dim3(GX, 2), blk, 0, stream>>>(
+    k_mgemm<128, (MF_BIAS | MF_LRELU | MF_COLSUM), 1><<<dim3(2, GX), blk, 0, stream>>>(
         H, 320, 320, cv3wb, cv3b, nullptr, nullptr, 0, nullptr, pooled, nullptr, nullptr);
 
-    k_const4<<<1, 256, 0, stream>>>(pooled, ow, ob, c4, invn);
-    k_out<<<cdivu((unsigned)N, 256), blk, 0, stream>>>(H, ow, c4, out, N);
-}
+    k_out2<<<NB, blk, 0, stream>>>(H, ow, ob, pooled, out, N, invn);
+}
```
